# Performance work log

Hardware: AMD Instinct MI355X
Metric: run time of the kernel (lower is better)

## Reference

```python
import jax, jax.numpy as jnp
import numpy as np
import math

D_MODEL = 512
NUM_HEADS = 8
B, S = 2, 4096


def setup_inputs() -> dict:
    key = jax.random.key(0)
    ks = jax.random.split(key, 11)
    d = D_MODEL
    sc = 1.0 / math.sqrt(d)
    return {
        "query": jax.random.normal(ks[0], (B, S, d), jnp.float32),
        "key": jax.random.normal(ks[1], (B, S, d), jnp.float32),
        "value": jax.random.normal(ks[2], (B, S, d), jnp.float32),
        "Wq": jax.random.normal(ks[3], (d, d), jnp.float32) * sc,
        "bq": jnp.zeros((d,), jnp.float32),
        "Wk": jax.random.normal(ks[4], (d, d), jnp.float32) * sc,
        "bk": jnp.zeros((d,), jnp.float32),
        "Wv": jax.random.normal(ks[5], (d, d), jnp.float32) * sc,
        "bv": jnp.zeros((d,), jnp.float32),
        "Wo": jax.random.normal(ks[6], (d, d), jnp.float32) * sc,
        "bo": jnp.zeros((d,), jnp.float32),
    }


def reference(query, key, value, Wq, bq, Wk, bk, Wv, bv, Wo, bo):
    b, q_len, d_model = query.shape
    k_len = key.shape[1]
    h = NUM_HEADS
    d_k = d_model // h
    q = (query @ Wq.T + bq).reshape(b, q_len, h, d_k)
    k = (key @ Wk.T + bk).reshape(b, k_len, h, d_k)
    v = (value @ Wv.T + bv).reshape(b, k_len, h, d_k)
    # NOTE: faithful to source — softmax WITHOUT pre-scaling, then divide by sqrt(d_k)
    comp = jnp.einsum('bqhd,bkhd->bhqk', q, k)
    attn = jax.nn.softmax(comp, axis=-1) / jnp.sqrt(jnp.asarray(d_k, comp.dtype))
    x = jnp.einsum('bhqk,bkhd->bqhd', attn, v)
    return x.reshape(b, q_len, d_model) @ Wo.T + bo
```

## Files before the change

### kernel.cpp

```cpp
#include <hip/hip_runtime.h>

typedef _Float16 f16;
typedef __fp16 fp16x2 __attribute__((ext_vector_type(2)));
typedef _Float16 half4 __attribute__((ext_vector_type(4)));
typedef _Float16 half8 __attribute__((ext_vector_type(8)));
typedef float f32x4 __attribute__((ext_vector_type(4)));
typedef float float4v __attribute__((ext_vector_type(4)));

#define LOG2E 1.44269504088896340736f

__device__ __forceinline__ half8 cat8(half4 a, half4 b) {
    half8 r;
    r[0] = a[0]; r[1] = a[1]; r[2] = a[2]; r[3] = a[3];
    r[4] = b[0]; r[5] = b[1]; r[6] = b[2]; r[7] = b[3];
    return r;
}

union H8 { fp16x2 h2[4]; half8 h8; };

#define TR8(baddr, d0,d1,d2,d3,d4,d5,d6,d7)                                   \
  asm volatile("ds_read_b64_tr_b16 %0, %8 offset:0\n\t"                       \
               "ds_read_b64_tr_b16 %1, %8 offset:512\n\t"                     \
               "ds_read_b64_tr_b16 %2, %8 offset:128\n\t"                     \
               "ds_read_b64_tr_b16 %3, %8 offset:640\n\t"                     \
               "ds_read_b64_tr_b16 %4, %8 offset:256\n\t"                     \
               "ds_read_b64_tr_b16 %5, %8 offset:768\n\t"                     \
               "ds_read_b64_tr_b16 %6, %8 offset:384\n\t"                     \
               "ds_read_b64_tr_b16 %7, %8 offset:896"                         \
               : "=&v"(d0),"=&v"(d1),"=&v"(d2),"=&v"(d3),                     \
                 "=&v"(d4),"=&v"(d5),"=&v"(d6),"=&v"(d7)                      \
               : "v"(baddr) : "memory")

#define LGKM0_FENCE()                                                          \
  do { asm volatile("s_waitcnt lgkmcnt(0)" ::: "memory");                      \
       __builtin_amdgcn_sched_barrier(0); } while (0)

__device__ __forceinline__ void softmax_pack(
    f32x4 sf[4], float& mL, float& l, f32x4 o[4], H8& pb0, H8& pb1)
{
    float vm01 = fmaxf(fmaxf(fmaxf(sf[0][0], sf[0][1]), fmaxf(sf[0][2], sf[0][3])),
                       fmaxf(fmaxf(sf[1][0], sf[1][1]), fmaxf(sf[1][2], sf[1][3])));
    float vm23 = fmaxf(fmaxf(fmaxf(sf[2][0], sf[2][1]), fmaxf(sf[2][2], sf[2][3])),
                       fmaxf(fmaxf(sf[3][0], sf[3][1]), fmaxf(sf[3][2], sf[3][3])));
    float vm = fmaxf(vm01, vm23);
    vm = fmaxf(vm, __shfl_xor(vm, 16, 64));
    vm = fmaxf(vm, __shfl_xor(vm, 32, 64));
    float vmL = vm * LOG2E;

    if (__any(vmL > mL + 8.0f)) {
        float mn = fmaxf(mL, vmL);
        float al = __builtin_amdgcn_exp2f(mL - mn);
        l *= al;
        #pragma unroll
        for (int db = 0; db < 4; ++db) o[db] *= al;
        mL = mn;
    }

    f32x4 pe[4];
    float rs = 0.0f;
    #pragma unroll
    for (int kb = 0; kb < 4; ++kb) {
        #pragma unroll
        for (int ro = 0; ro < 4; ++ro) {
            float p = __builtin_amdgcn_exp2f(fmaf(sf[kb][ro], LOG2E, -mL));
            pe[kb][ro] = p;
            rs += p;
        }
    }
    rs += __shfl_xor(rs, 16, 64);
    rs += __shfl_xor(rs, 32, 64);
    l += rs;

    pb0.h2[0] = __builtin_amdgcn_cvt_pkrtz(pe[0][0], pe[0][1]);
    pb0.h2[1] = __builtin_amdgcn_cvt_pkrtz(pe[0][2], pe[0][3]);
    pb0.h2[2] = __builtin_amdgcn_cvt_pkrtz(pe[1][0], pe[1][1]);
    pb0.h2[3] = __builtin_amdgcn_cvt_pkrtz(pe[1][2], pe[1][3]);
    pb1.h2[0] = __builtin_amdgcn_cvt_pkrtz(pe[2][0], pe[2][1]);
    pb1.h2[1] = __builtin_amdgcn_cvt_pkrtz(pe[2][2], pe[2][3]);
    pb1.h2[2] = __builtin_amdgcn_cvt_pkrtz(pe[3][0], pe[3][1]);
    pb1.h2[3] = __builtin_amdgcn_cvt_pkrtz(pe[3][2], pe[3][3]);
}

__global__ __launch_bounds__(256) void qkv_proj(
    const float* __restrict__ Aq, const float* __restrict__ Ak, const float* __restrict__ Av,
    const float* __restrict__ Wq, const float* __restrict__ Wk, const float* __restrict__ Wv,
    const float* __restrict__ bq, const float* __restrict__ bk, const float* __restrict__ bv,
    f16* __restrict__ Qh, f16* __restrict__ Kh, f16* __restrict__ Vh)
{
    const int z = blockIdx.z;
    const float* __restrict__ A    = (z == 0) ? Aq : (z == 1) ? Ak : Av;
    const float* __restrict__ W    = (z == 0) ? Wq : (z == 1) ? Wk : Wv;
    const float* __restrict__ bias = (z == 0) ? bq : (z == 1) ? bk : bv;
    f16* __restrict__ dst          = (z == 0) ? Qh : (z == 1) ? Kh : Vh;

    __shared__ __align__(16) f16 As[128 * 40];
    __shared__ __align__(16) f16 Ws[128 * 40];

    const int t  = threadIdx.x;
    const int m0 = blockIdx.y * 128;
    const int n0 = blockIdx.x * 128;
    const int w = t >> 6, lane = t & 63, lr = lane & 15, lg = lane >> 4;
    const int wr = w >> 1, wc = w & 1;

    f32x4 acc[4][4] = {};

    for (int k0 = 0; k0 < 512; k0 += 32) {
        #pragma unroll
        for (int it = 0; it < 2; ++it) {
            int c = t + it * 256;
            int row  = c >> 2;
            int col8 = (c & 3) * 8;

            const float* ga = A + (size_t)(m0 + row) * 512 + k0 + col8;
            float4v a0 = *(const float4v*)ga;
            float4v a1 = *(const float4v*)(ga + 4);
            half8 ha;
            ha[0] = (f16)a0[0]; ha[1] = (f16)a0[1]; ha[2] = (f16)a0[2]; ha[3] = (f16)a0[3];
            ha[4] = (f16)a1[0]; ha[5] = (f16)a1[1]; ha[6] = (f16)a1[2]; ha[7] = (f16)a1[3];
            *(half8*)&As[row * 40 + col8] = ha;

            const float* gw = W + (size_t)(n0 + row) * 512 + k0 + col8;
            float4v w0 = *(const float4v*)gw;
            float4v w1 = *(const float4v*)(gw + 4);
            half8 hw;
            hw[0] = (f16)w0[0]; hw[1] = (f16)w0[1]; hw[2] = (f16)w0[2]; hw[3] = (f16)w0[3];
            hw[4] = (f16)w1[0]; hw[5] = (f16)w1[1]; hw[6] = (f16)w1[2]; hw[7] = (f16)w1[3];
            *(half8*)&Ws[row * 40 + col8] = hw;
        }
        __syncthreads();

        half8 af[4], bf[4];
        #pragma unroll
        for (int i = 0; i < 4; ++i) {
            af[i] = *(const half8*)&As[(wr * 64 + i * 16 + lr) * 40 + lg * 8];
            bf[i] = *(const half8*)&Ws[(wc * 64 + i * 16 + lr) * 40 + lg * 8];
        }
        #pragma unroll
        for (int mi = 0; mi < 4; ++mi)
            #pragma unroll
            for (int ni = 0; ni < 4; ++ni)
                acc[mi][ni] = __builtin_amdgcn_mfma_f32_16x16x32_f16(af[mi], bf[ni], acc[mi][ni], 0, 0, 0);
        __syncthreads();
    }

    #pragma unroll
    for (int mi = 0; mi < 4; ++mi) {
        #pragma unroll
        for (int ni = 0; ni < 4; ++ni) {
            int col = n0 + wc * 64 + ni * 16 + lr;
            float bv_ = bias[col];
            int h  = col >> 6;
            int dd = col & 63;
            #pragma unroll
            for (int r = 0; r < 4; ++r) {
                int row = m0 + wr * 64 + mi * 16 + lg * 4 + r;
                int b = row >> 12;
                int s = row & 4095;
                dst[(((size_t)(b * 8 + h)) * 4096 + s) * 64 + dd] = (f16)(acc[mi][ni][r] + bv_);
            }
        }
    }
}

__global__ __launch_bounds__(256, 2) void flash_attn(
    const f16* __restrict__ Qh, const f16* __restrict__ Kh, const f16* __restrict__ Vh,
    f16* __restrict__ Xh)
{
    const int bh  = blockIdx.y;
    const int t = threadIdx.x, w = t >> 6, lane = t & 63, lr = lane & 15, lg = lane >> 4;
    const int q0 = blockIdx.x * 128 + w * 32;

    __shared__ __align__(16) f16 Ks[2][64 * 72];
    __shared__ __align__(16) f16 Vs[2][64 * 64];

    const size_t hb = (size_t)bh * (4096 * 64);

    half8 aq00 = *(const half8*)&Qh[hb + (size_t)(q0 + lr) * 64 + lg * 8];
    half8 aq01 = *(const half8*)&Qh[hb + (size_t)(q0 + lr) * 64 + 32 + lg * 8];
    half8 aq10 = *(const half8*)&Qh[hb + (size_t)(q0 + 16 + lr) * 64 + lg * 8];
    half8 aq11 = *(const half8*)&Qh[hb + (size_t)(q0 + 16 + lr) * 64 + 32 + lg * 8];

    const int srow = t >> 3;
    const int scol = (t & 7) * 8;
    const int kdstA = srow * 72 + scol;
    const int kdstB = kdstA + 32 * 72;
    const int vdstA = ((((srow >> 2) & 3) * 16) + (srow >> 4) * 4 + (scol >> 4)) * 64
                    + (srow & 3) * 16 + (scol & 15);
    const int vdstB = vdstA + 512;

    f32x4 o0[4] = {}, o1[4] = {};
    float mL0 = -INFINITY, l0 = 0.0f, mL1 = -INFINITY, l1 = 0.0f;

    const f16* kbase = Kh + hb + (size_t)srow * 64 + scol;
    const f16* vbase = Vh + hb + (size_t)srow * 64 + scol;

    half8 kregA = *(const half8*)kbase;
    half8 kregB = *(const half8*)(kbase + 2048);
    half8 vregA = *(const half8*)vbase;
    half8 vregB = *(const half8*)(vbase + 2048);

    for (int kt = 0; kt < 4096; kt += 64) {
        const int bi = (kt >> 6) & 1;
        f16* ks = &Ks[bi][0];
        f16* vs = &Vs[bi][0];

        *(half8*)&ks[kdstA] = kregA;
        *(half8*)&ks[kdstB] = kregB;
        *(half8*)&vs[vdstA] = vregA;
        *(half8*)&vs[vdstB] = vregB;
        __syncthreads();

        int koff = ((kt + 64) & 4095) << 6;
        kregA = *(const half8*)(kbase + koff);
        kregB = *(const half8*)(kbase + 2048 + koff);
        vregA = *(const half8*)(vbase + koff);
        vregB = *(const half8*)(vbase + 2048 + koff);

        f32x4 sf0[4] = {}, sf1[4] = {};
        #pragma unroll
        for (int c = 0; c < 2; ++c) {
            half8 kf[4];
            #pragma unroll
            for (int kb = 0; kb < 4; ++kb)
                kf[kb] = *(const half8*)&ks[(kb * 16 + lr) * 72 + c * 32 + lg * 8];
            half8 a0 = c ? aq01 : aq00;
            half8 a1 = c ? aq11 : aq10;
            __builtin_amdgcn_s_setprio(1);
            #pragma unroll
            for (int kb = 0; kb < 4; ++kb)
                sf0[kb] = __builtin_amdgcn_mfma_f32_16x16x32_f16(kf[kb], a0, sf0[kb], 0, 0, 0);
            #pragma unroll
            for (int kb = 0; kb < 4; ++kb)
                sf1[kb] = __builtin_amdgcn_mfma_f32_16x16x32_f16(kf[kb], a1, sf1[kb], 0, 0, 0);
            __builtin_amdgcn_s_setprio(0);
        }

        H8 p00, p01, p10, p11;
        softmax_pack(sf0, mL0, l0, o0, p00, p01);
        softmax_pack(sf1, mL1, l1, o1, p10, p11);

        const unsigned vb = (unsigned)(size_t)vs + (unsigned)(lg * 2048 + lr * 8);
        {
            half4 u0,u1,u2,u3,u4,u5,u6,u7;
            TR8(vb, u0,u1,u2,u3,u4,u5,u6,u7);
            LGKM0_FENCE();
            __builtin_amdgcn_s_setprio(1);
            o0[0] = __builtin_amdgcn_mfma_f32_16x16x32_f16(cat8(u0,u1), p00.h8, o0[0], 0, 0, 0);
            o0[1] = __builtin_amdgcn_mfma_f32_16x16x32_f16(cat8(u2,u3), p00.h8, o0[1], 0, 0, 0);
            o0[2] = __builtin_amdgcn_mfma_f32_16x16x32_f16(cat8(u4,u5), p00.h8, o0[2], 0, 0, 0);
            o0[3] = __builtin_amdgcn_mfma_f32_16x16x32_f16(cat8(u6,u7), p00.h8, o0[3], 0, 0, 0);
            o1[0] = __builtin_amdgcn_mfma_f32_16x16x32_f16(cat8(u0,u1), p10.h8, o1[0], 0, 0, 0);
            o1[1] = __builtin_amdgcn_mfma_f32_16x16x32_f16(cat8(u2,u3), p10.h8, o1[1], 0, 0, 0);
            o1[2] = __builtin_amdgcn_mfma_f32_16x16x32_f16(cat8(u4,u5), p10.h8, o1[2], 0, 0, 0);
            o1[3] = __builtin_amdgcn_mfma_f32_16x16x32_f16(cat8(u6,u7), p10.h8, o1[3], 0, 0, 0);
            __builtin_amdgcn_s_setprio(0);
            TR8(vb + 1024u, u0,u1,u2,u3,u4,u5,u6,u7);
            LGKM0_FENCE();
            __builtin_amdgcn_s_setprio(1);
            o0[0] = __builtin_amdgcn_mfma_f32_16x16x32_f16(cat8(u0,u1), p01.h8, o0[0], 0, 0, 0);
            o0[1] = __builtin_amdgcn_mfma_f32_16x16x32_f16(cat8(u2,u3), p01.h8, o0[1], 0, 0, 0);
            o0[2] = __builtin_amdgcn_mfma_f32_16x16x32_f16(cat8(u4,u5), p01.h8, o0[2], 0, 0, 0);
            o0[3] = __builtin_amdgcn_mfma_f32_16x16x32_f16(cat8(u6,u7), p01.h8, o0[3], 0, 0, 0);
            o1[0] = __builtin_amdgcn_mfma_f32_16x16x32_f16(cat8(u0,u1), p11.h8, o1[0], 0, 0, 0);
            o1[1] = __builtin_amdgcn_mfma_f32_16x16x32_f16(cat8(u2,u3), p11.h8, o1[1], 0, 0, 0);
            o1[2] = __builtin_amdgcn_mfma_f32_16x16x32_f16(cat8(u4,u5), p11.h8, o1[2], 0, 0, 0);
            o1[3] = __builtin_amdgcn_mfma_f32_16x16x32_f16(cat8(u6,u7), p11.h8, o1[3], 0, 0, 0);
            __builtin_amdgcn_s_setprio(0);
        }
    }

    const int b = bh >> 3, h = bh & 7;
    const float inv0 = 1.0f / (l0 * 8.0f);
    const float inv1 = 1.0f / (l1 * 8.0f);
    const int q0_ = q0 + lr, q1_ = q0 + 16 + lr;
    #pragma unroll
    for (int db = 0; db < 4; ++db) {
        half4 hv0, hv1;
        hv0[0] = (f16)(o0[db][0] * inv0);
        hv0[1] = (f16)(o0[db][1] * inv0);
        hv0[2] = (f16)(o0[db][2] * inv0);
        hv0[3] = (f16)(o0[db][3] * inv0);
        *(half4*)&Xh[((size_t)(b * 4096 + q0_)) * 512 + h * 64 + db * 16 + lg * 4] = hv0;
        hv1[0] = (f16)(o1[db][0] * inv1);
        hv1[1] = (f16)(o1[db][1] * inv1);
        hv1[2] = (f16)(o1[db][2] * inv1);
        hv1[3] = (f16)(o1[db][3] * inv1);
        *(half4*)&Xh[((size_t)(b * 4096 + q1_)) * 512 + h * 64 + db * 16 + lg * 4] = hv1;
    }
}

__global__ __launch_bounds__(256) void out_proj(
    const f16* __restrict__ Xh, const float* __restrict__ Wo, const float* __restrict__ bo,
    float* __restrict__ out)
{
    __shared__ __align__(16) f16 As[128 * 40];
    __shared__ __align__(16) f16 Ws[128 * 40];

    const int t  = threadIdx.x;
    const int m0 = blockIdx.y * 128;
    const int n0 = blockIdx.x * 128;
    const int w = t >> 6, lane = t & 63, lr = lane & 15, lg = lane >> 4;
    const int wr = w >> 1, wc = w & 1;

    f32x4 acc[4][4] = {};

    for (int k0 = 0; k0 < 512; k0 += 32) {
        #pragma unroll
        for (int it = 0; it < 2; ++it) {
            int c = t + it * 256;
            int row  = c >> 2;
            int col8 = (c & 3) * 8;

            *(half8*)&As[row * 40 + col8] =
                *(const half8*)&Xh[(size_t)(m0 + row) * 512 + k0 + col8];

            const float* gw = Wo + (size_t)(n0 + row) * 512 + k0 + col8;
            float4v w0 = *(const float4v*)gw;
            float4v w1 = *(const float4v*)(gw + 4);
            half8 hw;
            hw[0] = (f16)w0[0]; hw[1] = (f16)w0[1]; hw[2] = (f16)w0[2]; hw[3] = (f16)w0[3];
            hw[4] = (f16)w1[0]; hw[5] = (f16)w1[1]; hw[6] = (f16)w1[2]; hw[7] = (f16)w1[3];
            *(half8*)&Ws[row * 40 + col8] = hw;
        }
        __syncthreads();

        half8 af[4], bf[4];
        #pragma unroll
        for (int i = 0; i < 4; ++i) {
            af[i] = *(const half8*)&As[(wr * 64 + i * 16 + lr) * 40 + lg * 8];
            bf[i] = *(const half8*)&Ws[(wc * 64 + i * 16 + lr) * 40 + lg * 8];
        }
        #pragma unroll
        for (int mi = 0; mi < 4; ++mi)
            #pragma unroll
            for (int ni = 0; ni < 4; ++ni)
                acc[mi][ni] = __builtin_amdgcn_mfma_f32_16x16x32_f16(af[mi], bf[ni], acc[mi][ni], 0, 0, 0);
        __syncthreads();
    }

    #pragma unroll
    for (int mi = 0; mi < 4; ++mi) {
        #pragma unroll
        for (int ni = 0; ni < 4; ++ni) {
            int col = n0 + wc * 64 + ni * 16 + lr;
            float bb = bo[col];
            #pragma unroll
            for (int r = 0; r < 4; ++r) {
                int row = m0 + wr * 64 + mi * 16 + lg * 4 + r;
                out[(size_t)row * 512 + col] = acc[mi][ni][r] + bb;
            }
        }
    }
}

extern "C" void kernel_launch(void* const* d_in, const int* in_sizes, int n_in,
                              void* d_out, int out_size, void* d_ws, size_t ws_size,
                              hipStream_t stream) {
    const float* query = (const float*)d_in[0];
    const float* key   = (const float*)d_in[1];
    const float* value = (const float*)d_in[2];
    const float* Wq    = (const float*)d_in[3];
    const float* bq    = (const float*)d_in[4];
    const float* Wk    = (const float*)d_in[5];
    const float* bk    = (const float*)d_in[6];
    const float* Wv    = (const float*)d_in[7];
    const float* bv    = (const float*)d_in[8];
    const float* Wo    = (const float*)d_in[9];
    const float* bo    = (const float*)d_in[10];
    float* out = (float*)d_out;

    char* ws = (char*)d_ws;
    f16* Qh = (f16*)(ws);
    f16* Kh = (f16*)(ws + 8388608);
    f16* Vh = (f16*)(ws + 16777216);
    f16* Xh = (f16*)(ws + 25165824);

    qkv_proj<<<dim3(4, 64, 3), 256, 0, stream>>>(query, key, value,
                                                 Wq, Wk, Wv, bq, bk, bv,
                                                 Qh, Kh, Vh);
    flash_attn<<<dim3(32, 16), 256, 0, stream>>>(Qh, Kh, Vh, Xh);
    out_proj<<<dim3(4, 64), 256, 0, stream>>>(Xh, Wo, bo, out);
}
```

Baseline: 169.3 us.

## Compute softmax row sums with MFMA against ones and hoist V transposed reads

Replaces the per-lane scalar row-sum accumulation and its cross-lane shuffles with extra MFMA instructions that multiply the fp16 probabilities by a ones vector, accumulating the denominator in the matrix unit. Both V transposed LDS reads are now issued before the exponentials so their latency overlaps softmax work, and a single LDS wait replaces the two previous ones. The first QK MFMA starts from a zero constant instead of zero-initialized accumulators. The row sum now uses fp16-rounded probabilities rather than fp32 values, and holding both V fragments at once raises register pressure.

```diff
diff --git a/kernel.cpp b/kernel.cpp
--- a/kernel.cpp
+++ b/kernel.cpp
@@ -35,50 +35,48 @@
   do { asm volatile("s_waitcnt lgkmcnt(0)" ::: "memory");                      \
        __builtin_amdgcn_sched_barrier(0); } while (0)
 
-__device__ __forceinline__ void softmax_pack(
-    f32x4 sf[4], float& mL, float& l, f32x4 o[4], H8& pb0, H8& pb1)
+__device__ __forceinline__ float rowmax16(const f32x4 sf[4]) {
+    float a = fmaxf(fmaxf(sf[0][0], sf[0][1]), fmaxf(sf[0][2], sf[0][3]));
+    float b = fmaxf(fmaxf(sf[1][0], sf[1][1]), fmaxf(sf[1][2], sf[1][3]));
+    float c = fmaxf(fmaxf(sf[2][0], sf[2][1]), fmaxf(sf[2][2], sf[2][3]));
+    float d = fmaxf(fmaxf(sf[3][0], sf[3][1]), fmaxf(sf[3][2], sf[3][3]));
+    return fmaxf(fmaxf(a, b), fmaxf(c, d));
+}
+
+__device__ __forceinline__ void max_defer(
+    const f32x4 sf[4], float& mL, f32x4 o[4], f32x4& la)
 {
-    float vm01 = fmaxf(fmaxf(fmaxf(sf[0][0], sf[0][1]), fmaxf(sf[0][2], sf[0][3])),
-                       fmaxf(fmaxf(sf[1][0], sf[1][1]), fmaxf(sf[1][2], sf[1][3])));
-    float vm23 = fmaxf(fmaxf(fmaxf(sf[2][0], sf[2][1]), fmaxf(sf[2][2], sf[2][3])),
-                       fmaxf(fmaxf(sf[3][0], sf[3][1]), fmaxf(sf[3][2], sf[3][3])));
-    float vm = fmaxf(vm01, vm23);
+    float vm = rowmax16(sf);
     vm = fmaxf(vm, __shfl_xor(vm, 16, 64));
     vm = fmaxf(vm, __shfl_xor(vm, 32, 64));
     float vmL = vm * LOG2E;
-
     if (__any(vmL > mL + 8.0f)) {
         float mn = fmaxf(mL, vmL);
         float al = __builtin_amdgcn_exp2f(mL - mn);
-        l *= al;
+        la *= al;
         #pragma unroll
         for (int db = 0; db < 4; ++db) o[db] *= al;
         mL = mn;
     }
-
-    f32x4 pe[4];
-    float rs = 0.0f;
+}
+
+__device__ __forceinline__ void exp_pack(
+    const f32x4 sf[4], float mL, H8& pb0, H8& pb1)
+{
+    float pe[16];
     #pragma unroll
-    for (int kb = 0; kb < 4; ++kb) {
-        #pragma unroll
-        for (int ro = 0; ro < 4; ++ro) {
-            float p = __builtin_amdgcn_exp2f(fmaf(sf[kb][ro], LOG2E, -mL));
-            pe[kb][ro] = p;
-            rs += p;
-        }
-    }
-    rs += __shfl_xor(rs, 16, 64);
-    rs += __shfl_xor(rs, 32, 64);
-    l += rs;
-
-    pb0.h2[0] = __builtin_amdgcn_cvt_pkrtz(pe[0][0], pe[0][1]);
-    pb0.h2[1] = __builtin_amdgcn_cvt_pkrtz(pe[0][2], pe[0][3]);
-    pb0.h2[2] = __builtin_amdgcn_cvt_pkrtz(pe[1][0], pe[1][1]);
-    pb0.h2[3] = __builtin_amdgcn_cvt_pkrtz(pe[1][2], pe[1][3]);
-    pb1.h2[0] = __builtin_amdgcn_cvt_pkrtz(pe[2][0], pe[2][1]);
-    pb1.h2[1] = __builtin_amdgcn_cvt_pkrtz(pe[2][2], pe[2][3]);
-    pb1.h2[2] = __builtin_amdgcn_cvt_pkrtz(pe[3][0], pe[3][1]);
-    pb1.h2[3] = __builtin_amdgcn_cvt_pkrtz(pe[3][2], pe[3][3]);
+    for (int kb = 0; kb < 4; ++kb)
+        #pragma unroll
+        for (int ro = 0; ro < 4; ++ro)
+            pe[kb * 4 + ro] = __builtin_amdgcn_exp2f(fmaf(sf[kb][ro], LOG2E, -mL));
+    pb0.h2[0] = __builtin_amdgcn_cvt_pkrtz(pe[0],  pe[1]);
+    pb0.h2[1] = __builtin_amdgcn_cvt_pkrtz(pe[2],  pe[3]);
+    pb0.h2[2] = __builtin_amdgcn_cvt_pkrtz(pe[4],  pe[5]);
+    pb0.h2[3] = __builtin_amdgcn_cvt_pkrtz(pe[6],  pe[7]);
+    pb1.h2[0] = __builtin_amdgcn_cvt_pkrtz(pe[8],  pe[9]);
+    pb1.h2[1] = __builtin_amdgcn_cvt_pkrtz(pe[10], pe[11]);
+    pb1.h2[2] = __builtin_amdgcn_cvt_pkrtz(pe[12], pe[13]);
+    pb1.h2[3] = __builtin_amdgcn_cvt_pkrtz(pe[14], pe[15]);
 }
 
 __global__ __launch_bounds__(256) void qkv_proj(
@@ -180,6 +178,11 @@
     half8 aq10 = *(const half8*)&Qh[hb + (size_t)(q0 + 16 + lr) * 64 + lg * 8];
     half8 aq11 = *(const half8*)&Qh[hb + (size_t)(q0 + 16 + lr) * 64 + 32 + lg * 8];
 
+    half8 ones;
+    #pragma unroll
+    for (int j = 0; j < 8; ++j) ones[j] = (f16)1.0f;
+    const f32x4 zf = {0.0f, 0.0f, 0.0f, 0.0f};
+
     const int srow = t >> 3;
     const int scol = (t & 7) * 8;
     const int kdstA = srow * 72 + scol;
@@ -189,7 +192,8 @@
     const int vdstB = vdstA + 512;
 
     f32x4 o0[4] = {}, o1[4] = {};
-    float mL0 = -INFINITY, l0 = 0.0f, mL1 = -INFINITY, l1 = 0.0f;
+    f32x4 la0 = {}, la1 = {};
+    float mL0 = -INFINITY, mL1 = -INFINITY;
 
     const f16* kbase = Kh + hb + (size_t)srow * 64 + scol;
     const f16* vbase = Vh + hb + (size_t)srow * 64 + scol;
@@ -216,62 +220,75 @@
         vregA = *(const half8*)(vbase + koff);
         vregB = *(const half8*)(vbase + 2048 + koff);
 
-        f32x4 sf0[4] = {}, sf1[4] = {};
-        #pragma unroll
-        for (int c = 0; c < 2; ++c) {
+        f32x4 sf0[4], sf1[4];
+        {
             half8 kf[4];
             #pragma unroll
             for (int kb = 0; kb < 4; ++kb)
-                kf[kb] = *(const half8*)&ks[(kb * 16 + lr) * 72 + c * 32 + lg * 8];
-            half8 a0 = c ? aq01 : aq00;
-            half8 a1 = c ? aq11 : aq10;
+                kf[kb] = *(const half8*)&ks[(kb * 16 + lr) * 72 + lg * 8];
             __builtin_amdgcn_s_setprio(1);
             #pragma unroll
             for (int kb = 0; kb < 4; ++kb)
-                sf0[kb] = __builtin_amdgcn_mfma_f32_16x16x32_f16(kf[kb], a0, sf0[kb], 0, 0, 0);
-            #pragma unroll
-            for (int kb = 0; kb < 4; ++kb)
-                sf1[kb] = __builtin_amdgcn_mfma_f32_16x16x32_f16(kf[kb], a1, sf1[kb], 0, 0, 0);
+                sf0[kb] = __builtin_amdgcn_mfma_f32_16x16x32_f16(kf[kb], aq00, zf, 0, 0, 0);
+            #pragma unroll
+            for (int kb = 0; kb < 4; ++kb)
+                sf1[kb] = __builtin_amdgcn_mfma_f32_16x16x32_f16(kf[kb], aq10, zf, 0, 0, 0);
             __builtin_amdgcn_s_setprio(0);
-        }
+            #pragma unroll
+            for (int kb = 0; kb < 4; ++kb)
+                kf[kb] = *(const half8*)&ks[(kb * 16 + lr) * 72 + 32 + lg * 8];
+            __builtin_amdgcn_s_setprio(1);
+            #pragma unroll
+            for (int kb = 0; kb < 4; ++kb)
+                sf0[kb] = __builtin_amdgcn_mfma_f32_16x16x32_f16(kf[kb], aq01, sf0[kb], 0, 0, 0);
+            #pragma unroll
+            for (int kb = 0; kb < 4; ++kb)
+                sf1[kb] = __builtin_amdgcn_mfma_f32_16x16x32_f16(kf[kb], aq11, sf1[kb], 0, 0, 0);
+            __builtin_amdgcn_s_setprio(0);
+        }
+
+        max_defer(sf0, mL0, o0, la0);
+        max_defer(sf1, mL1, o1, la1);
+
+        const unsigned vb = (unsigned)(size_t)vs + (unsigned)(lg * 2048 + lr * 8);
+        half4 ua0,ua1,ua2,ua3,ua4,ua5,ua6,ua7;
+        half4 ub0,ub1,ub2,ub3,ub4,ub5,ub6,ub7;
+        TR8(vb,         ua0,ua1,ua2,ua3,ua4,ua5,ua6,ua7);
+        TR8(vb + 1024u, ub0,ub1,ub2,ub3,ub4,ub5,ub6,ub7);
 
         H8 p00, p01, p10, p11;
-        softmax_pack(sf0, mL0, l0, o0, p00, p01);
-        softmax_pack(sf1, mL1, l1, o1, p10, p11);
-
-        const unsigned vb = (unsigned)(size_t)vs + (unsigned)(lg * 2048 + lr * 8);
-        {
-            half4 u0,u1,u2,u3,u4,u5,u6,u7;
-            TR8(vb, u0,u1,u2,u3,u4,u5,u6,u7);
-            LGKM0_FENCE();
-            __builtin_amdgcn_s_setprio(1);
-            o0[0] = __builtin_amdgcn_mfma_f32_16x16x32_f16(cat8(u0,u1), p00.h8, o0[0], 0, 0, 0);
-            o0[1] = __builtin_amdgcn_mfma_f32_16x16x32_f16(cat8(u2,u3), p00.h8, o0[1], 0, 0, 0);
-            o0[2] = __builtin_amdgcn_mfma_f32_16x16x32_f16(cat8(u4,u5), p00.h8, o0[2], 0, 0, 0);
-            o0[3] = __builtin_amdgcn_mfma_f32_16x16x32_f16(cat8(u6,u7), p00.h8, o0[3], 0, 0, 0);
-            o1[0] = __builtin_amdgcn_mfma_f32_16x16x32_f16(cat8(u0,u1), p10.h8, o1[0], 0, 0, 0);
-            o1[1] = __builtin_amdgcn_mfma_f32_16x16x32_f16(cat8(u2,u3), p10.h8, o1[1], 0, 0, 0);
-            o1[2] = __builtin_amdgcn_mfma_f32_16x16x32_f16(cat8(u4,u5), p10.h8, o1[2], 0, 0, 0);
-            o1[3] = __builtin_amdgcn_mfma_f32_16x16x32_f16(cat8(u6,u7), p10.h8, o1[3], 0, 0, 0);
-            __builtin_amdgcn_s_setprio(0);
-            TR8(vb + 1024u, u0,u1,u2,u3,u4,u5,u6,u7);
-            LGKM0_FENCE();
-            __builtin_amdgcn_s_setprio(1);
-            o0[0] = __builtin_amdgcn_mfma_f32_16x16x32_f16(cat8(u0,u1), p01.h8, o0[0], 0, 0, 0);
-            o0[1] = __builtin_amdgcn_mfma_f32_16x16x32_f16(cat8(u2,u3), p01.h8, o0[1], 0, 0, 0);
-            o0[2] = __builtin_amdgcn_mfma_f32_16x16x32_f16(cat8(u4,u5), p01.h8, o0[2], 0, 0, 0);
-            o0[3] = __builtin_amdgcn_mfma_f32_16x16x32_f16(cat8(u6,u7), p01.h8, o0[3], 0, 0, 0);
-            o1[0] = __builtin_amdgcn_mfma_f32_16x16x32_f16(cat8(u0,u1), p11.h8, o1[0], 0, 0, 0);
-            o1[1] = __builtin_amdgcn_mfma_f32_16x16x32_f16(cat8(u2,u3), p11.h8, o1[1], 0, 0, 0);
-            o1[2] = __builtin_amdgcn_mfma_f32_16x16x32_f16(cat8(u4,u5), p11.h8, o1[2], 0, 0, 0);
-            o1[3] = __builtin_amdgcn_mfma_f32_16x16x32_f16(cat8(u6,u7), p11.h8, o1[3], 0, 0, 0);
-            __builtin_amdgcn_s_setprio(0);
-        }
+        exp_pack(sf0, mL0, p00, p01);
+        exp_pack(sf1, mL1, p10, p11);
+
+        LGKM0_FENCE();
+
+        __builtin_amdgcn_s_setprio(1);
+        o0[0] = __builtin_amdgcn_mfma_f32_16x16x32_f16(cat8(ua0,ua1), p00.h8, o0[0], 0, 0, 0);
+        o0[1] = __builtin_amdgcn_mfma_f32_16x16x32_f16(cat8(ua2,ua3), p00.h8, o0[1], 0, 0, 0);
+        o0[2] = __builtin_amdgcn_mfma_f32_16x16x32_f16(cat8(ua4,ua5), p00.h8, o0[2], 0, 0, 0);
+        o0[3] = __builtin_amdgcn_mfma_f32_16x16x32_f16(cat8(ua6,ua7), p00.h8, o0[3], 0, 0, 0);
+        o1[0] = __builtin_amdgcn_mfma_f32_16x16x32_f16(cat8(ua0,ua1), p10.h8, o1[0], 0, 0, 0);
+        o1[1] = __builtin_amdgcn_mfma_f32_16x16x32_f16(cat8(ua2,ua3), p10.h8, o1[1], 0, 0, 0);
+        o1[2] = __builtin_amdgcn_mfma_f32_16x16x32_f16(cat8(ua4,ua5), p10.h8, o1[2], 0, 0, 0);
+        o1[3] = __builtin_amdgcn_mfma_f32_16x16x32_f16(cat8(ua6,ua7), p10.h8, o1[3], 0, 0, 0);
+        la0 = __builtin_amdgcn_mfma_f32_16x16x32_f16(ones, p00.h8, la0, 0, 0, 0);
+        la1 = __builtin_amdgcn_mfma_f32_16x16x32_f16(ones, p10.h8, la1, 0, 0, 0);
+        o0[0] = __builtin_amdgcn_mfma_f32_16x16x32_f16(cat8(ub0,ub1), p01.h8, o0[0], 0, 0, 0);
+        o0[1] = __builtin_amdgcn_mfma_f32_16x16x32_f16(cat8(ub2,ub3), p01.h8, o0[1], 0, 0, 0);
+        o0[2] = __builtin_amdgcn_mfma_f32_16x16x32_f16(cat8(ub4,ub5), p01.h8, o0[2], 0, 0, 0);
+        o0[3] = __builtin_amdgcn_mfma_f32_16x16x32_f16(cat8(ub6,ub7), p01.h8, o0[3], 0, 0, 0);
+        o1[0] = __builtin_amdgcn_mfma_f32_16x16x32_f16(cat8(ub0,ub1), p11.h8, o1[0], 0, 0, 0);
+        o1[1] = __builtin_amdgcn_mfma_f32_16x16x32_f16(cat8(ub2,ub3), p11.h8, o1[1], 0, 0, 0);
+        o1[2] = __builtin_amdgcn_mfma_f32_16x16x32_f16(cat8(ub4,ub5), p11.h8, o1[2], 0, 0, 0);
+        o1[3] = __builtin_amdgcn_mfma_f32_16x16x32_f16(cat8(ub6,ub7), p11.h8, o1[3], 0, 0, 0);
+        la0 = __builtin_amdgcn_mfma_f32_16x16x32_f16(ones, p01.h8, la0, 0, 0, 0);
+        la1 = __builtin_amdgcn_mfma_f32_16x16x32_f16(ones, p11.h8, la1, 0, 0, 0);
+        __builtin_amdgcn_s_setprio(0);
     }
 
     const int b = bh >> 3, h = bh & 7;
-    const float inv0 = 1.0f / (l0 * 8.0f);
-    const float inv1 = 1.0f / (l1 * 8.0f);
+    const float inv0 = 1.0f / (la0[0] * 8.0f);
+    const float inv1 = 1.0f / (la1[0] * 8.0f);
     const int q0_ = q0 + lr, q1_ = q0 + 16 + lr;
     #pragma unroll
     for (int db = 0; db < 4; ++db) {
```

After: 164.6 us. -2.8%, faster.
